# Optimization experiments

Hardware: AMD Instinct MI355X
Metric: run time of the kernel (lower is better)

The kernel has to match this reference:

```python
import jax, jax.numpy as jnp
import numpy as np

N = 10000   # nodes
E = 80000   # edges per graph (avg degree 8)
H = 32      # hidden width (hard-coded in module)
VD0 = 2048  # visual_dim for gcn_0
VD1 = 256   # visual_dim // 8 for gcn_b21


def setup_inputs() -> dict:
    key = jax.random.key(0)
    ks = jax.random.split(key, 16)
    rn = lambda k, s, sc=1.0: jax.random.normal(k, s, dtype=jnp.float32) * sc
    return {
        "x": rn(ks[0], (N, 9)),
        "vis0": rn(ks[1], (N, VD0)),
        "vis1": rn(ks[2], (N, VD1)),
        "edge_index0": jax.random.randint(ks[3], (2, E), 0, N),
        "edge_index1": jax.random.randint(ks[4], (2, E), 0, N),
        # input_mlp: Linear(9,32) -> BatchNorm1d(32) (eval) -> PReLU -> Dropout(0) -> Linear(32,32)
        "W_in1": rn(ks[5], (9, H), 0.3), "b_in1": jnp.zeros((H,), jnp.float32),
        "bn_gamma": jnp.ones((H,), jnp.float32), "bn_beta": jnp.zeros((H,), jnp.float32),
        "bn_mean": jnp.zeros((H,), jnp.float32), "bn_var": jnp.ones((H,), jnp.float32),
        "prelu_a": jnp.asarray(0.25, jnp.float32),
        "W_in2": rn(ks[6], (H, H), 0.15), "b_in2": jnp.zeros((H,), jnp.float32),
        "w_node": rn(ks[7], (H, 1), 0.15), "b_node": jnp.zeros((1,), jnp.float32),
        "W_c0": rn(ks[8], (H, H), 0.15), "b_c0": jnp.zeros((H,), jnp.float32),
        "W_c1": rn(ks[9], (H, H), 0.15), "b_c1": jnp.zeros((H,), jnp.float32),
        "w_p0": rn(ks[10], (H, 1), 0.15), "b_p0": jnp.zeros((1,), jnp.float32),
        "w_p1": rn(ks[11], (H, 1), 0.15), "b_p1": jnp.zeros((1,), jnp.float32),
    }


def _cm_cos_conv(h, edge_index, vis, W, b):
    # gather-weight-scatter: w_e = cos(vis[src], vis[dst]); out_i = (sum_e->i w_e * h[src_e]) @ W + b
    src, dst = edge_index[0], edge_index[1]
    vn = vis * jax.lax.rsqrt(jnp.sum(vis * vis, axis=-1, keepdims=True) + 1e-8)
    w = jnp.sum(vn[src] * vn[dst], axis=-1)  # [E] cosine similarity per edge
    agg = jax.ops.segment_sum(h[src] * w[:, None], dst, num_segments=h.shape[0])  # [N,H]
    return agg @ W + b  # conv_activation=None -> identity


def reference(x, vis0, vis1, edge_index0, edge_index1, W_in1, b_in1, bn_gamma, bn_beta, bn_mean, bn_var, prelu_a, W_in2, b_in2, w_node, b_node, W_c0, b_c0, W_c1, b_c1, w_p0, b_p0, w_p1, b_p1):
    h = x @ W_in1 + b_in1
    h = bn_gamma * (h - bn_mean) * jax.lax.rsqrt(bn_var + 1e-5) + bn_beta
    h = jnp.where(h >= 0, h, prelu_a * h)  # PReLU (single shared slope)
    h = h @ W_in2 + b_in2                   # [N,32] shared for graphs 0 and 4
    nodes_scores = (h @ w_node + b_node)[:, 0]
    h0 = _cm_cos_conv(h, edge_index0, vis0, W_c0, b_c0)
    h1 = _cm_cos_conv(h, edge_index1, vis1, W_c1, b_c1)
    s0 = (h0 @ w_p0 + b_p0)[:, 0]
    s1 = (h1 @ w_p1 + b_p1)[:, 0]
    return nodes_scores + s0 + s1
```

## Files before the change

kernel.cpp:

```cpp
#include <hip/hip_runtime.h>

#define N_NODES 10000
#define NE      80000
#define H       32
#define VD0     2048
#define VD1     256

#define EDGE_CAP 32

#define ZERO_BLOCKS 79
#define A_MLP    40
#define A_NC0    2500
#define A_NC1    2500
#define A_UNITS  (A_MLP + A_NC0 + A_NC1)

#define C_PHASES 8
#define C_G0     (C_PHASES * 2500)
#define C_UNITS  (C_G0 + 2500)

__device__ inline unsigned short f2bf_rne(float f) {
    unsigned int u = __float_as_uint(f);
    u += 0x7fffu + ((u >> 16) & 1u);
    return (unsigned short)(u >> 16);
}
__device__ inline float bflo(unsigned int u) { return __uint_as_float(u << 16); }
__device__ inline float bfhi(unsigned int u) { return __uint_as_float(u & 0xffff0000u); }
__device__ inline float bfs(unsigned short u) { return __uint_as_float((unsigned int)u << 16); }

__device__ inline float dot4_bf16(uint2 a, uint2 b) {
    return bflo(a.x) * bflo(b.x) + bfhi(a.x) * bfhi(b.x)
         + bflo(a.y) * bflo(b.y) + bfhi(a.y) * bfhi(b.y);
}

struct KP {
    const float* x;
    const float* vis0; const float* vis1;
    const int* ei0; const int* ei1;
    const float* W_in1; const float* b_in1;
    const float* bn_gamma; const float* bn_beta;
    const float* bn_mean; const float* bn_var;
    const float* prelu_a;
    const float* W_in2; const float* b_in2;
    const float* w_node; const float* b_node;
    const float* W_c0; const float* b_c0;
    const float* W_c1; const float* b_c1;
    const float* w_p0; const float* b_p0;
    const float* w_p1; const float* b_p1;
    float* out; float* p0w; float* p1w;
    unsigned short* vn0; unsigned short* vn1;
    uint2* b0; uint2* b1;
    int* cur0; int* cur1;
};

template <int VD>
__device__ inline void normconv_node(const float* __restrict__ vis,
                                     unsigned short* __restrict__ vn,
                                     int node, int lane)
{
    const float4* v = (const float4*)(vis + (size_t)node * VD);
    float4 f[VD / 256];
    float acc = 0.f;
    #pragma unroll
    for (int it = 0; it < VD / 256; it++) {
        f[it] = v[it * 64 + lane];
        acc += f[it].x * f[it].x + f[it].y * f[it].y + f[it].z * f[it].z + f[it].w * f[it].w;
    }
    #pragma unroll
    for (int o = 32; o; o >>= 1) acc += __shfl_xor(acc, o);
    const float inv = rsqrtf(acc + 1e-8f);
    ushort4* o4 = (ushort4*)(vn + (size_t)node * VD);
    #pragma unroll
    for (int it = 0; it < VD / 256; it++) {
        ushort4 r;
        r.x = f2bf_rne(f[it].x * inv);
        r.y = f2bf_rne(f[it].y * inv);
        r.z = f2bf_rne(f[it].z * inv);
        r.w = f2bf_rne(f[it].w * inv);
        o4[it * 64 + lane] = r;
    }
}

__device__ inline void stageA_unit(const KP& p, int u, int t)
{
    if (u < A_MLP) {
        __shared__ float sW1[9 * H];
        __shared__ float sW2[H * H];
        __shared__ float sU0[H], sU1[H], sWn[H];
        __shared__ float sB1[H], sB2[H], sSc[H], sSh[H];
        __shared__ float sC;

        for (int i = t; i < 9 * H; i += 256) sW1[i] = p.W_in1[i];
        for (int i = t; i < H * H; i += 256) sW2[i] = p.W_in2[i];
        if (t < H) {
            sB1[t] = p.b_in1[t];
            sB2[t] = p.b_in2[t];
            float sc = p.bn_gamma[t] * rsqrtf(p.bn_var[t] + 1e-5f);
            sSc[t] = sc;
            sSh[t] = p.bn_beta[t] - p.bn_mean[t] * sc;
            sWn[t] = p.w_node[t];
            float u0 = 0.f, u1 = 0.f;
            for (int j = 0; j < H; j++) {
                u0 += p.W_c0[t * H + j] * p.w_p0[j];
                u1 += p.W_c1[t * H + j] * p.w_p1[j];
            }
            sU0[t] = u0; sU1[t] = u1;
        }
        if (t == 0) {
            float c0 = p.b_p0[0], c1 = p.b_p1[0];
            for (int j = 0; j < H; j++) { c0 += p.b_c0[j] * p.w_p0[j]; c1 += p.b_c1[j] * p.w_p1[j]; }
            sC = c0 + c1 + p.b_node[0];
        }
        __syncthreads();

        const float a = p.prelu_a[0];
        const int n = u * 256 + t;
        if (n < N_NODES) {
            float xi[9];
            #pragma unroll
            for (int i = 0; i < 9; i++) xi[i] = p.x[n * 9 + i];

            float tt[H];
            #pragma unroll
            for (int j = 0; j < H; j++) {
                float s = sB1[j];
                #pragma unroll
                for (int i = 0; i < 9; i++) s += xi[i] * sW1[i * H + j];
                s = s * sSc[j] + sSh[j];
                tt[j] = s >= 0.f ? s : a * s;
            }

            float ns = 0.f, p0 = 0.f, p1 = 0.f;
            #pragma unroll
            for (int k = 0; k < H; k++) {
                float h = sB2[k];
                #pragma unroll
                for (int j = 0; j < H; j++) h += tt[j] * sW2[j * H + k];
                ns += h * sWn[k];
                p0 += h * sU0[k];
                p1 += h * sU1[k];
            }
            p.out[n] = ns + sC;
            p.p0w[n] = p0;
            p.p1w[n] = p1;
        }
    } else if (u < A_MLP + A_NC0) {
        const int node = (u - A_MLP) * 4 + (t >> 6);
        normconv_node<VD0>(p.vis0, p.vn0, node, t & 63);
    } else {
        const int node = (u - A_MLP - A_NC0) * 4 + (t >> 6);
        normconv_node<VD1>(p.vis1, p.vn1, node, t & 63);
    }
}

__device__ inline void stageB_edge(const KP& p, int e)
{
    {
        const int s = p.ei0[e];
        const int d = p.ei0[NE + e];
        const int pos = atomicAdd(&p.cur0[d], 1);
        if (pos < EDGE_CAP) {
            p.b0[d * EDGE_CAP + pos] = make_uint2((unsigned)(s * (VD0 * 2)),
                                                  __float_as_uint(p.p0w[s]));
        } else {
            const unsigned short* a = p.vn0 + (size_t)s * VD0;
            const unsigned short* c = p.vn0 + (size_t)d * VD0;
            float acc = 0.f;
            for (int i = 0; i < VD0; i++) acc += bfs(a[i]) * bfs(c[i]);
            atomicAdd(&p.out[d], acc * p.p0w[s]);
        }
    }
    {
        const int s = p.ei1[e];
        const int d = p.ei1[NE + e];
        const int pos = atomicAdd(&p.cur1[d], 1);
        if (pos < EDGE_CAP) {
            p.b1[d * EDGE_CAP + pos] = make_uint2((unsigned)(s * (VD1 * 2)),
                                                  __float_as_uint(p.p1w[s]));
        } else {
            const unsigned short* a = p.vn1 + (size_t)s * VD1;
            const unsigned short* c = p.vn1 + (size_t)d * VD1;
            float acc = 0.f;
            for (int i = 0; i < VD1; i++) acc += bfs(a[i]) * bfs(c[i]);
            atomicAdd(&p.out[d], acc * p.p1w[s]);
        }
    }
}

__device__ inline void stageC_unit(const KP& p, int u, int t)
{
    const int lane = t & 63;

    if (u < C_G0) {
        const int phase = u & 7;
        const int group = u >> 3;
        const int d     = group * 4 + (t >> 6);
        int cnt = p.cur0[d];
        if (cnt <= 0) return;
        cnt = cnt < EDGE_CAP ? cnt : EDGE_CAP;
        const int last = cnt - 1;

        const char* base = (const char*)p.vn0;
        const int koffB  = phase * 512 + lane * 8;
        const uint2 dreg = *(const uint2*)(base + d * (VD0 * 2) + koffB);
        const uint2* eb  = p.b0 + d * EDGE_CAP;

        float partial = 0.f;
        for (int j = 0; j < cnt; j += 8) {
            uint2 e[8];
            #pragma unroll
            for (int k = 0; k < 8; k++) {
                int jj = j + k;
                jj = jj > last ? last : jj;
                e[k] = eb[jj];
            }
            uint2 r[8];
            #pragma unroll
            for (int k = 0; k < 8; k++)
                r[k] = *(const uint2*)(base + e[k].x + koffB);
            #pragma unroll
            for (int k = 0; k < 8; k++) {
                const float pw = (j + k <= last) ? __uint_as_float(e[k].y) : 0.f;
                partial += dot4_bf16(dreg, r[k]) * pw;
            }
        }
        #pragma unroll
        for (int o = 32; o; o >>= 1) partial += __shfl_down(partial, o);
        if (lane == 0) atomicAdd(&p.out[d], partial);
    } else {
        const int d = (u - C_G0) * 4 + (t >> 6);
        int cnt = p.cur1[d];
        if (cnt <= 0) return;
        cnt = cnt < EDGE_CAP ? cnt : EDGE_CAP;
        const int last = cnt - 1;

        const char* base = (const char*)p.vn1;
        const int koffB  = lane * 8;
        const uint2 dreg = *(const uint2*)(base + d * (VD1 * 2) + koffB);
        const uint2* eb  = p.b1 + d * EDGE_CAP;

        float partial = 0.f;
        for (int j = 0; j < cnt; j += 8) {
            uint2 e[8];
            #pragma unroll
            for (int k = 0; k < 8; k++) {
                int jj = j + k;
                jj = jj > last ? last : jj;
                e[k] = eb[jj];
            }
            uint2 r[8];
            #pragma unroll
            for (int k = 0; k < 8; k++)
                r[k] = *(const uint2*)(base + e[k].x + koffB);
            #pragma unroll
            for (int k = 0; k < 8; k++) {
                const float pw = (j + k <= last) ? __uint_as_float(e[k].y) : 0.f;
                partial += dot4_bf16(dreg, r[k]) * pw;
            }
        }
        #pragma unroll
        for (int o = 32; o; o >>= 1) partial += __shfl_down(partial, o);
        if (lane == 0) atomicAdd(&p.out[d], partial);
    }
}

__global__ __launch_bounds__(256) void prep2_kernel(KP p)
{
    const int b = blockIdx.x, t = threadIdx.x;
    if (b < ZERO_BLOCKS) {
        const int i = b * 256 + t;
        if (i < 2 * N_NODES) p.cur0[i] = 0;
    } else {
        stageA_unit(p, b - ZERO_BLOCKS, t);
    }
}
__global__ __launch_bounds__(256) void scatter2_kernel(KP p)
{
    const int e = blockIdx.x * 256 + threadIdx.x;
    if (e < NE) stageB_edge(p, e);
}
__global__ __launch_bounds__(256) void edge2_kernel(KP p)
{
    stageC_unit(p, blockIdx.x, threadIdx.x);
}

template <int VD>
__global__ __launch_bounds__(256) void norm_kernel(const float* __restrict__ vis,
                                                   float* __restrict__ inv)
{
    const int wave = (blockIdx.x * 256 + threadIdx.x) >> 6;
    const int lane = threadIdx.x & 63;
    if (wave >= N_NODES) return;
    const float4* v = (const float4*)(vis + (size_t)wave * VD);
    float acc = 0.f;
    #pragma unroll
    for (int it = 0; it < VD / 256; it++) {
        float4 f = v[lane + it * 64];
        acc += f.x * f.x + f.y * f.y + f.z * f.z + f.w * f.w;
    }
    #pragma unroll
    for (int o = 32; o; o >>= 1) acc += __shfl_down(acc, o);
    if (lane == 0) inv[wave] = rsqrtf(acc + 1e-8f);
}

template <int VD>
__global__ __launch_bounds__(256) void edge_kernel(
    const float* __restrict__ vis, const int* __restrict__ ei,
    const float* __restrict__ inv, const float* __restrict__ pz,
    float* __restrict__ out)
{
    const int wave = (blockIdx.x * 256 + threadIdx.x) >> 6;
    const int lane = threadIdx.x & 63;
    if (wave >= NE) return;
    const int src = ei[wave];
    const int dst = ei[NE + wave];
    const float4* va = (const float4*)(vis + (size_t)src * VD);
    const float4* vb = (const float4*)(vis + (size_t)dst * VD);
    float acc = 0.f;
    #pragma unroll
    for (int it = 0; it < VD / 256; it++) {
        float4 fa = va[lane + it * 64];
        float4 fb = vb[lane + it * 64];
        acc += fa.x * fb.x + fa.y * fb.y + fa.z * fb.z + fa.w * fb.w;
    }
    #pragma unroll
    for (int o = 32; o; o >>= 1) acc += __shfl_down(acc, o);
    if (lane == 0) {
        float w = acc * inv[src] * inv[dst];
        atomicAdd(&out[dst], w * pz[src]);
    }
}

__global__ __launch_bounds__(256) void node_kernel_fb(KP p)
{
    stageA_unit(p, (int)blockIdx.x, (int)threadIdx.x);
}

extern "C" void kernel_launch(void* const* d_in, const int* in_sizes, int n_in,
                              void* d_out, int out_size, void* d_ws, size_t ws_size,
                              hipStream_t stream)
{
    KP hp;
    hp.x        = (const float*)d_in[0];
    hp.vis0     = (const float*)d_in[1];
    hp.vis1     = (const float*)d_in[2];
    hp.ei0      = (const int*)d_in[3];
    hp.ei1      = (const int*)d_in[4];
    hp.W_in1    = (const float*)d_in[5];
    hp.b_in1    = (const float*)d_in[6];
    hp.bn_gamma = (const float*)d_in[7];
    hp.bn_beta  = (const float*)d_in[8];
    hp.bn_mean  = (const float*)d_in[9];
    hp.bn_var   = (const float*)d_in[10];
    hp.prelu_a  = (const float*)d_in[11];
    hp.W_in2    = (const float*)d_in[12];
    hp.b_in2    = (const float*)d_in[13];
    hp.w_node   = (const float*)d_in[14];
    hp.b_node   = (const float*)d_in[15];
    hp.W_c0     = (const float*)d_in[16];
    hp.b_c0     = (const float*)d_in[17];
    hp.W_c1     = (const float*)d_in[18];
    hp.b_c1     = (const float*)d_in[19];
    hp.w_p0     = (const float*)d_in[20];
    hp.b_p0     = (const float*)d_in[21];
    hp.w_p1     = (const float*)d_in[22];
    hp.b_p1     = (const float*)d_in[23];
    hp.out      = (float*)d_out;

    char* ws = (char*)d_ws;
    hp.p0w  = (float*)ws;                  ws += N_NODES * 4;
    hp.p1w  = (float*)ws;                  ws += N_NODES * 4;
    float* inv0 = (float*)ws;              ws += N_NODES * 4;
    float* inv1 = (float*)ws;              ws += N_NODES * 4;
    hp.vn0  = (unsigned short*)ws;         ws += (size_t)N_NODES * VD0 * 2;
    hp.vn1  = (unsigned short*)ws;         ws += (size_t)N_NODES * VD1 * 2;
    hp.b0   = (uint2*)ws;                  ws += (size_t)N_NODES * EDGE_CAP * 8;
    hp.b1   = (uint2*)ws;                  ws += (size_t)N_NODES * EDGE_CAP * 8;
    hp.cur0 = (int*)ws;                    ws += N_NODES * 4;
    hp.cur1 = (int*)ws;                    ws += N_NODES * 4;
    const size_t need = (size_t)(ws - (char*)d_ws);

    if (ws_size >= need) {
        prep2_kernel<<<ZERO_BLOCKS + A_UNITS, 256, 0, stream>>>(hp);
        scatter2_kernel<<<(NE + 255) / 256, 256, 0, stream>>>(hp);
        edge2_kernel<<<C_UNITS, 256, 0, stream>>>(hp);
    } else {
        node_kernel_fb<<<A_MLP, 256, 0, stream>>>(hp);
        norm_kernel<VD0><<<(N_NODES * 64 + 255) / 256, 256, 0, stream>>>(hp.vis0, inv0);
        norm_kernel<VD1><<<(N_NODES * 64 + 255) / 256, 256, 0, stream>>>(hp.vis1, inv1);
        edge_kernel<VD0><<<(NE * 64 + 255) / 256, 256, 0, stream>>>(hp.vis0, hp.ei0, inv0, hp.p0w, hp.out);
        edge_kernel<VD1><<<(NE * 64 + 255) / 256, 256, 0, stream>>>(hp.vis1, hp.ei1, inv1, hp.p1w, hp.out);
    }
}
```

Measured before the change: 261.1 us.

## Merge scatter into prep kernel, batch destinations per wave, defer overflow edges

The edge scatter stage now runs in the same launch as the node MLP and normalisation, and counters are cleared with a memset, removing one kernel launch. Because the scatter can run before the MLP has written p0w/p1w, the bucket entries store the source index and p0w/p1w is looked up later in the edge kernel. The edge kernel gives each wave several destination nodes in turn, prefetches the next node's count and vector slice, and loads 16 edges at a time. Edges beyond the bucket capacity go to an overflow list that dedicated blocks handle with wave-parallel dot products, replacing the slow per-thread serial fallback. Giving each wave several destinations can leave the GPU with less parallelism.

```diff
diff --git a/kernel.cpp b/kernel.cpp
--- a/kernel.cpp
+++ b/kernel.cpp
@@ -8,15 +8,18 @@
 
 #define EDGE_CAP 32
 
-#define ZERO_BLOCKS 79
+#define S_BLOCKS 313
 #define A_MLP    40
 #define A_NC0    2500
 #define A_NC1    2500
-#define A_UNITS  (A_MLP + A_NC0 + A_NC1)
-
-#define C_PHASES 8
-#define C_G0     (C_PHASES * 2500)
-#define C_UNITS  (C_G0 + 2500)
+#define PREP_BLOCKS (S_BLOCKS + A_MLP + A_NC0 + A_NC1)
+
+#define E_G0BLK  2000
+#define DPW0     10
+#define E_G1BLK  500
+#define DPW1     5
+#define OVF_BLOCKS 16
+#define EDGE_BLOCKS (E_G0BLK + E_G1BLK + OVF_BLOCKS)
 
 __device__ inline unsigned short f2bf_rne(float f) {
     unsigned int u = __float_as_uint(f);
@@ -25,11 +28,21 @@
 }
 __device__ inline float bflo(unsigned int u) { return __uint_as_float(u << 16); }
 __device__ inline float bfhi(unsigned int u) { return __uint_as_float(u & 0xffff0000u); }
-__device__ inline float bfs(unsigned short u) { return __uint_as_float((unsigned int)u << 16); }
-
+
+__device__ inline float dot8_bf16(uint4 a, uint4 b) {
+    float s;
+    s  = bflo(a.x) * bflo(b.x) + bfhi(a.x) * bfhi(b.x);
+    s += bflo(a.y) * bflo(b.y) + bfhi(a.y) * bfhi(b.y);
+    s += bflo(a.z) * bflo(b.z) + bfhi(a.z) * bfhi(b.z);
+    s += bflo(a.w) * bflo(b.w) + bfhi(a.w) * bfhi(b.w);
+    return s;
+}
 __device__ inline float dot4_bf16(uint2 a, uint2 b) {
     return bflo(a.x) * bflo(b.x) + bfhi(a.x) * bfhi(b.x)
          + bflo(a.y) * bflo(b.y) + bfhi(a.y) * bfhi(b.y);
+}
+__device__ inline float dot4_pre(float a0, float a1, float a2, float a3, uint2 b) {
+    return a0 * bflo(b.x) + a1 * bfhi(b.x) + a2 * bflo(b.y) + a3 * bfhi(b.y);
 }
 
 struct KP {
@@ -49,7 +62,8 @@
     float* out; float* p0w; float* p1w;
     unsigned short* vn0; unsigned short* vn1;
     uint2* b0; uint2* b1;
-    int* cur0; int* cur1;
+    int2* ovf0; int2* ovf1;
+    int* cur0; int* cur1; int* ovfn;
 };
 
 template <int VD>
@@ -158,129 +172,145 @@
         const int s = p.ei0[e];
         const int d = p.ei0[NE + e];
         const int pos = atomicAdd(&p.cur0[d], 1);
-        if (pos < EDGE_CAP) {
-            p.b0[d * EDGE_CAP + pos] = make_uint2((unsigned)(s * (VD0 * 2)),
-                                                  __float_as_uint(p.p0w[s]));
-        } else {
-            const unsigned short* a = p.vn0 + (size_t)s * VD0;
-            const unsigned short* c = p.vn0 + (size_t)d * VD0;
-            float acc = 0.f;
-            for (int i = 0; i < VD0; i++) acc += bfs(a[i]) * bfs(c[i]);
-            atomicAdd(&p.out[d], acc * p.p0w[s]);
-        }
+        if (pos < EDGE_CAP)
+            p.b0[d * EDGE_CAP + pos] = make_uint2((unsigned)(s * (VD0 * 2)), (unsigned)s);
+        else
+            p.ovf0[atomicAdd(&p.ovfn[0], 1)] = make_int2(d, s);
     }
     {
         const int s = p.ei1[e];
         const int d = p.ei1[NE + e];
         const int pos = atomicAdd(&p.cur1[d], 1);
-        if (pos < EDGE_CAP) {
-            p.b1[d * EDGE_CAP + pos] = make_uint2((unsigned)(s * (VD1 * 2)),
-                                                  __float_as_uint(p.p1w[s]));
-        } else {
-            const unsigned short* a = p.vn1 + (size_t)s * VD1;
-            const unsigned short* c = p.vn1 + (size_t)d * VD1;
-            float acc = 0.f;
-            for (int i = 0; i < VD1; i++) acc += bfs(a[i]) * bfs(c[i]);
-            atomicAdd(&p.out[d], acc * p.p1w[s]);
-        }
-    }
-}
-
-__device__ inline void stageC_unit(const KP& p, int u, int t)
-{
+        if (pos < EDGE_CAP)
+            p.b1[d * EDGE_CAP + pos] = make_uint2((unsigned)(s * (VD1 * 2)), (unsigned)s);
+        else
+            p.ovf1[atomicAdd(&p.ovfn[1], 1)] = make_int2(d, s);
+    }
+}
+
+__device__ inline float chunk16(const char* __restrict__ base,
+                                const float* __restrict__ pwv,
+                                const uint2* __restrict__ eb, int j, int c,
+                                int koffB, float a0, float a1, float a2, float a3)
+{
+    uint2 e[16];
+    #pragma unroll
+    for (int k = 0; k < 16; k++) {
+        uint2 tt = eb[j + k];
+        e[k] = (j + k < c) ? tt : make_uint2(0u, 0u);
+    }
+    uint2 r[16];
+    #pragma unroll
+    for (int k = 0; k < 16; k++)
+        r[k] = *(const uint2*)(base + e[k].x + koffB);
+    float s = 0.f;
+    #pragma unroll
+    for (int k = 0; k < 16; k++) {
+        float pw = pwv[e[k].y];
+        pw = (j + k < c) ? pw : 0.f;
+        s += dot4_pre(a0, a1, a2, a3, r[k]) * pw;
+    }
+    return s;
+}
+
+__global__ __launch_bounds__(256, 3) void edge3_kernel(KP p)
+{
+    const int bid  = blockIdx.x;
+    const int t    = threadIdx.x;
     const int lane = t & 63;
-
-    if (u < C_G0) {
-        const int phase = u & 7;
-        const int group = u >> 3;
-        const int d     = group * 4 + (t >> 6);
-        int cnt = p.cur0[d];
-        if (cnt <= 0) return;
-        cnt = cnt < EDGE_CAP ? cnt : EDGE_CAP;
-        const int last = cnt - 1;
-
+    const int warp = t >> 6;
+
+    if (bid < E_G0BLK) {
+        const int phase = bid & 7;
+        const int q     = bid >> 3;
+        const int wv    = q * 4 + warp;
+        const int d0 = wv * DPW0, d1 = d0 + DPW0;
         const char* base = (const char*)p.vn0;
         const int koffB  = phase * 512 + lane * 8;
-        const uint2 dreg = *(const uint2*)(base + d * (VD0 * 2) + koffB);
-        const uint2* eb  = p.b0 + d * EDGE_CAP;
-
-        float partial = 0.f;
-        for (int j = 0; j < cnt; j += 8) {
-            uint2 e[8];
-            #pragma unroll
-            for (int k = 0; k < 8; k++) {
-                int jj = j + k;
-                jj = jj > last ? last : jj;
-                e[k] = eb[jj];
-            }
-            uint2 r[8];
-            #pragma unroll
-            for (int k = 0; k < 8; k++)
-                r[k] = *(const uint2*)(base + e[k].x + koffB);
-            #pragma unroll
-            for (int k = 0; k < 8; k++) {
-                const float pw = (j + k <= last) ? __uint_as_float(e[k].y) : 0.f;
-                partial += dot4_bf16(dreg, r[k]) * pw;
-            }
-        }
-        #pragma unroll
-        for (int o = 32; o; o >>= 1) partial += __shfl_down(partial, o);
-        if (lane == 0) atomicAdd(&p.out[d], partial);
-    } else {
-        const int d = (u - C_G0) * 4 + (t >> 6);
-        int cnt = p.cur1[d];
-        if (cnt <= 0) return;
-        cnt = cnt < EDGE_CAP ? cnt : EDGE_CAP;
-        const int last = cnt - 1;
-
+
+        int cnt = p.cur0[d0];
+        uint2 dreg = *(const uint2*)(base + (size_t)d0 * (VD0 * 2) + koffB);
+        for (int d = d0; d < d1; d++) {
+            const int c = cnt < EDGE_CAP ? cnt : EDGE_CAP;
+            const uint2* eb = p.b0 + (size_t)d * EDGE_CAP;
+            const int dn = (d + 1 < d1) ? d + 1 : d;
+            const int cnt_n = p.cur0[dn];
+            const uint2 dreg_n = *(const uint2*)(base + (size_t)dn * (VD0 * 2) + koffB);
+
+            const float a0 = bflo(dreg.x), a1 = bfhi(dreg.x);
+            const float a2 = bflo(dreg.y), a3 = bfhi(dreg.y);
+            float partial = chunk16(base, p.p0w, eb, 0, c, koffB, a0, a1, a2, a3);
+            if (c > 16)
+                partial += chunk16(base, p.p0w, eb, 16, c, koffB, a0, a1, a2, a3);
+
+            #pragma unroll
+            for (int o = 32; o; o >>= 1) partial += __shfl_down(partial, o);
+            if (lane == 0 && c > 0) atomicAdd(&p.out[d], partial);
+            cnt = cnt_n; dreg = dreg_n;
+        }
+    } else if (bid < E_G0BLK + E_G1BLK) {
+        const int wv = (bid - E_G0BLK) * 4 + warp;
+        const int d0 = wv * DPW1, d1 = d0 + DPW1;
         const char* base = (const char*)p.vn1;
         const int koffB  = lane * 8;
-        const uint2 dreg = *(const uint2*)(base + d * (VD1 * 2) + koffB);
-        const uint2* eb  = p.b1 + d * EDGE_CAP;
-
-        float partial = 0.f;
-        for (int j = 0; j < cnt; j += 8) {
-            uint2 e[8];
-            #pragma unroll
-            for (int k = 0; k < 8; k++) {
-                int jj = j + k;
-                jj = jj > last ? last : jj;
-                e[k] = eb[jj];
-            }
-            uint2 r[8];
-            #pragma unroll
-            for (int k = 0; k < 8; k++)
-                r[k] = *(const uint2*)(base + e[k].x + koffB);
-            #pragma unroll
-            for (int k = 0; k < 8; k++) {
-                const float pw = (j + k <= last) ? __uint_as_float(e[k].y) : 0.f;
-                partial += dot4_bf16(dreg, r[k]) * pw;
-            }
-        }
-        #pragma unroll
-        for (int o = 32; o; o >>= 1) partial += __shfl_down(partial, o);
-        if (lane == 0) atomicAdd(&p.out[d], partial);
-    }
-}
-
-__global__ __launch_bounds__(256) void prep2_kernel(KP p)
+
+        int cnt = p.cur1[d0];
+        uint2 dreg = *(const uint2*)(base + (size_t)d0 * (VD1 * 2) + koffB);
+        for (int d = d0; d < d1; d++) {
+            const int c = cnt < EDGE_CAP ? cnt : EDGE_CAP;
+            const uint2* eb = p.b1 + (size_t)d * EDGE_CAP;
+            const int dn = (d + 1 < d1) ? d + 1 : d;
+            const int cnt_n = p.cur1[dn];
+            const uint2 dreg_n = *(const uint2*)(base + (size_t)dn * (VD1 * 2) + koffB);
+
+            const float a0 = bflo(dreg.x), a1 = bfhi(dreg.x);
+            const float a2 = bflo(dreg.y), a3 = bfhi(dreg.y);
+            float partial = chunk16(base, p.p1w, eb, 0, c, koffB, a0, a1, a2, a3);
+            if (c > 16)
+                partial += chunk16(base, p.p1w, eb, 16, c, koffB, a0, a1, a2, a3);
+
+            #pragma unroll
+            for (int o = 32; o; o >>= 1) partial += __shfl_down(partial, o);
+            if (lane == 0 && c > 0) atomicAdd(&p.out[d], partial);
+            cnt = cnt_n; dreg = dreg_n;
+        }
+    } else {
+        const int wv = (bid - E_G0BLK - E_G1BLK) * 4 + warp;
+        const int n0 = p.ovfn[0];
+        for (int i = wv; i < n0; i += OVF_BLOCKS * 4) {
+            const int2 ds = p.ovf0[i];
+            const uint4* A = (const uint4*)(p.vn0 + (size_t)ds.y * VD0);
+            const uint4* B = (const uint4*)(p.vn0 + (size_t)ds.x * VD0);
+            float acc = 0.f;
+            #pragma unroll
+            for (int it = 0; it < 4; it++)
+                acc += dot8_bf16(A[it * 64 + lane], B[it * 64 + lane]);
+            #pragma unroll
+            for (int o = 32; o; o >>= 1) acc += __shfl_down(acc, o);
+            if (lane == 0) atomicAdd(&p.out[ds.x], acc * p.p0w[ds.y]);
+        }
+        const int n1 = p.ovfn[1];
+        for (int i = wv; i < n1; i += OVF_BLOCKS * 4) {
+            const int2 ds = p.ovf1[i];
+            const uint2* A = (const uint2*)(p.vn1 + (size_t)ds.y * VD1);
+            const uint2* B = (const uint2*)(p.vn1 + (size_t)ds.x * VD1);
+            float acc = dot4_bf16(A[lane], B[lane]);
+            #pragma unroll
+            for (int o = 32; o; o >>= 1) acc += __shfl_down(acc, o);
+            if (lane == 0) atomicAdd(&p.out[ds.x], acc * p.p1w[ds.y]);
+        }
+    }
+}
+
+__global__ __launch_bounds__(256) void prep3_kernel(KP p)
 {
     const int b = blockIdx.x, t = threadIdx.x;
-    if (b < ZERO_BLOCKS) {
-        const int i = b * 256 + t;
-        if (i < 2 * N_NODES) p.cur0[i] = 0;
+    if (b < S_BLOCKS) {
+        const int e = b * 256 + t;
+        if (e < NE) stageB_edge(p, e);
     } else {
-        stageA_unit(p, b - ZERO_BLOCKS, t);
-    }
-}
-__global__ __launch_bounds__(256) void scatter2_kernel(KP p)
-{
-    const int e = blockIdx.x * 256 + threadIdx.x;
-    if (e < NE) stageB_edge(p, e);
-}
-__global__ __launch_bounds__(256) void edge2_kernel(KP p)
-{
-    stageC_unit(p, blockIdx.x, threadIdx.x);
+        stageA_unit(p, b - S_BLOCKS, t);
+    }
 }
 
 template <int VD>
@@ -375,14 +405,17 @@
     hp.vn1  = (unsigned short*)ws;         ws += (size_t)N_NODES * VD1 * 2;
     hp.b0   = (uint2*)ws;                  ws += (size_t)N_NODES * EDGE_CAP * 8;
     hp.b1   = (uint2*)ws;                  ws += (size_t)N_NODES * EDGE_CAP * 8;
+    hp.ovf0 = (int2*)ws;                   ws += (size_t)NE * 8;
+    hp.ovf1 = (int2*)ws;                   ws += (size_t)NE * 8;
     hp.cur0 = (int*)ws;                    ws += N_NODES * 4;
     hp.cur1 = (int*)ws;                    ws += N_NODES * 4;
+    hp.ovfn = (int*)ws;                    ws += 16;
     const size_t need = (size_t)(ws - (char*)d_ws);
 
     if (ws_size >= need) {
-        prep2_kernel<<<ZERO_BLOCKS + A_UNITS, 256, 0, stream>>>(hp);
-        scatter2_kernel<<<(NE + 255) / 256, 256, 0, stream>>>(hp);
-        edge2_kernel<<<C_UNITS, 256, 0, stream>>>(hp);
+        hipMemsetAsync(hp.cur0, 0, 2 * N_NODES * sizeof(int) + 16, stream);
+        prep3_kernel<<<PREP_BLOCKS, 256, 0, stream>>>(hp);
+        edge3_kernel<<<EDGE_BLOCKS, 256, 0, stream>>>(hp);
     } else {
         node_kernel_fb<<<A_MLP, 256, 0, stream>>>(hp);
         norm_kernel<VD0><<<(N_NODES * 64 + 255) / 256, 256, 0, stream>>>(hp.vis0, inv0);
```

Result: slower. 296.7 us (+13.7%).
